# Optimization experiments

Measured on AMD Instinct MI355X. Metric: run time of the kernel, lower is better.

Reference implementation:

```python
import math
import jax, jax.numpy as jnp
import numpy as np

QDEPTH = 8
WIDTH = 32
HEIGHT = 32
PIXELS = WIDTH * HEIGHT          # 1024
WIRES = int(math.ceil(math.log2(PIXELS)))  # 10, and PIXELS == 2**WIRES exactly
BATCH = 2048


def setup_inputs() -> dict:
    key = jax.random.key(0)
    k1, k2 = jax.random.split(key)
    x = jax.random.normal(k1, (BATCH, 1, WIDTH, HEIGHT), dtype=jnp.float32)
    # torch.randn(weight_shape) * 0.4
    weights = jax.random.normal(k2, (QDEPTH, WIRES, 3), dtype=jnp.float32) * 0.4
    return {"x": x, "weights": weights, "reps": 1}


def _apply_1q(s, U, wire):
    # s: (batch, 2, 2, ..., 2); apply 2x2 unitary U on qubit `wire` (axis wire+1)
    ax = wire + 1
    s = jnp.moveaxis(s, ax, -1)
    s = s @ U.T                      # new[..., i] = sum_j U[i, j] * old[..., j]
    return jnp.moveaxis(s, -1, ax)


def _apply_cnot(s, ctrl, tgt):
    # flip target bit on the control==1 half of the state
    c_ax = ctrl + 1
    t_ax = tgt + 1
    s0 = jnp.take(s, 0, axis=c_ax)
    s1 = jnp.take(s, 1, axis=c_ax)
    t = t_ax - 1 if t_ax > c_ax else t_ax
    s1 = jnp.flip(s1, axis=t)
    return jnp.stack([s0, s1], axis=c_ax)


def _rot_matrix(phi, theta, omega):
    # qml.Rot = RZ(phi) -> RY(theta) -> RZ(omega)
    c = jnp.cos(theta * 0.5)
    sn = jnp.sin(theta * 0.5)
    ep = jnp.exp(-0.5j * (phi + omega))   # e^{-i(phi+omega)/2}
    em = jnp.exp(-0.5j * (phi - omega))   # e^{-i(phi-omega)/2}
    return jnp.stack([
        jnp.stack([ep * c, -jnp.conj(em) * sn]),
        jnp.stack([em * sn, jnp.conj(ep) * c]),
    ]).astype(jnp.complex64)


def _circuit(psi, weights, reps):
    # psi: (batch, 2**WIRES) complex64 normalized state
    b = psi.shape[0]
    s = psi.reshape((b,) + (2,) * WIRES)
    w = jnp.tanh(weights)                 # qw_map.tanh
    # StronglyEntanglingLayers default ranges: r_l = l % (wires-1) + 1
    ranges = [(l % (WIRES - 1)) + 1 for l in range(QDEPTH)]
    for _ in range(reps):
        for l in range(QDEPTH):
            for q in range(WIRES):
                U = _rot_matrix(w[l, q, 0], w[l, q, 1], w[l, q, 2])
                s = _apply_1q(s, U, q)
            r = ranges[l]
            for q in range(WIRES):
                s = _apply_cnot(s, q, (q + r) % WIRES)
    return s.reshape(b, 2 ** WIRES)


def reference(x, weights, reps):
    b = x.shape[0]
    v = x.reshape(b, PIXELS)                       # b 1 w h -> b (w h)
    old_norm = jnp.linalg.norm(v, axis=-1, keepdims=True)
    psi = (v / old_norm).astype(jnp.complex64)     # real amplitudes, zero imag
    out = _circuit(psi, weights, reps)
    out = out * old_norm.astype(jnp.complex64)
    return out.reshape(b, 1, WIDTH, HEIGHT)
```

## Files before the change

kernel.cpp:

```cpp
#include <hip/hip_runtime.h>
#include <math.h>


#define WIRES   10
#define NSTATE  1024
#define QDEPTH  8
#define NBATCH  2048
#define NGATES  (QDEPTH * WIRES)

typedef float v2f __attribute__((ext_vector_type(2)));
typedef unsigned int v2u __attribute__((ext_vector_type(2)));
static __device__ __forceinline__ v2f s2(float x) { return (v2f){x, x}; }

__device__ __forceinline__ int perm_g(int j, int r) {
#pragma unroll
    for (int q = WIRES - 1; q >= 0; --q) {
        const int cb = 9 - q;
        const int tb = 9 - ((q + r) % WIRES);
        j ^= ((j >> cb) & 1) << tb;
    }
    return j;
}

#if __has_builtin(__builtin_amdgcn_readlane)
static __device__ __forceinline__ int rli(int v, int idx) {
    return __builtin_amdgcn_readlane(v, idx);
}
#else
static __device__ __forceinline__ int rli(int v, int idx) {
    return __shfl(v, idx, 64);
}
#endif
static __device__ __forceinline__ float rlf(float v, int idx) {
    return __int_as_float(rli(__float_as_int(v), idx));
}

template<int CTRL>
__device__ __forceinline__ float dppmov(float x) {
    return __int_as_float(__builtin_amdgcn_update_dpp(
        0, __float_as_int(x), CTRL, 0xF, 0xF, true));
}
#define FX1(v)  dppmov<0xB1>(v)
#define FX2(v)  dppmov<0x4E>(v)
#define FX4(v)  dppmov<0x1B>(dppmov<0x141>(v))
#define FX8(v)  dppmov<0x128>(v)

#if __has_builtin(__builtin_amdgcn_permlane16_swap)
static __device__ __forceinline__ float pl16swap(float x) {
    const v2u r = __builtin_amdgcn_permlane16_swap(
        __float_as_uint(x), __float_as_uint(x), false, false);
    return __uint_as_float((threadIdx.x & 16) ? r.x : r.y);
}
#define FX16(v) pl16swap(v)
#else
#define FX16(v) __shfl_xor((v), 16, 64)
#endif

#if __has_builtin(__builtin_amdgcn_permlane32_swap)
static __device__ __forceinline__ float pl32swap(float x) {
    const v2u r = __builtin_amdgcn_permlane32_swap(
        __float_as_uint(x), __float_as_uint(x), false, false);
    return __uint_as_float((threadIdx.x & 32) ? r.x : r.y);
}
#define FX32(v) pl32swap(v)
#else
#define FX32(v) __shfl_xor((v), 32, 64)
#endif

__device__ __forceinline__ void gate_coeffs4(
    const float* __restrict__ w, int g, float (&c4)[4])
{
    const float phi   = tanhf(w[g * 3 + 0]);
    const float theta = tanhf(w[g * 3 + 1]);
    const float omega = tanhf(w[g * 3 + 2]);
    const float c  = cosf(theta * 0.5f);
    const float sn = sinf(theta * 0.5f);
    const float a  = 0.5f * (phi + omega);
    const float bb = 0.5f * (phi - omega);
    const float ca = cosf(a),  sa = sinf(a);
    const float cb = cosf(bb), sb = sinf(bb);
    c4[0] =  ca * c;
    c4[1] = -sa * c;
    c4[2] = -cb * sn;
    c4[3] = -sb * sn;
}

static __device__ __forceinline__ float sgnxor(float v, unsigned s) {
    return __uint_as_float(__float_as_uint(v) ^ s);
}

#define LOCAL_GATE(Q, MASK)                                                   \
    {                                                                         \
        const float u00r=getc(Q,0), u00i=getc(Q,1);                           \
        const float u01r=getc(Q,2), u01i=getc(Q,3);                           \
        _Pragma("unroll")                                                     \
        for (int k0 = 0; k0 < 8; ++k0) {                                      \
            if (k0 & (MASK)) continue;                                        \
            const int k1 = k0 | (MASK);                                       \
            const v2f a0r = zr[k0], a0i = zi[k0];                             \
            const v2f a1r = zr[k1], a1i = zi[k1];                             \
            zr[k0] = s2(u00r)*a0r - s2(u00i)*a0i + s2(u01r)*a1r - s2(u01i)*a1i;\
            zi[k0] = s2(u00r)*a0i + s2(u00i)*a0r + s2(u01r)*a1i + s2(u01i)*a1r;\
            zr[k1] = s2(u00r)*a1r + s2(u00i)*a1i - s2(u01r)*a0r - s2(u01i)*a0i;\
            zi[k1] = s2(u00r)*a1i - s2(u00i)*a1r - s2(u01r)*a0i + s2(u01i)*a0r;\
        }                                                                     \
    }

#define HSWAP_GATE(Q)                                                         \
    {                                                                         \
        const float u00r=getc(Q,0), u00i=getc(Q,1);                           \
        const float u01r=getc(Q,2), u01i=getc(Q,3);                           \
        const v2f pAr = s2(u00r);                                             \
        const v2f pAi = (v2f){u00i, -u00i};                                   \
        const v2f pBr = (v2f){u01r, -u01r};                                   \
        const v2f pBi = s2(u01i);                                             \
        _Pragma("unroll")                                                     \
        for (int k = 0; k < 8; ++k) {                                         \
            const v2f r  = zr[k], i = zi[k];                                  \
            const v2f rs = __builtin_shufflevector(r, r, 1, 0);               \
            const v2f is = __builtin_shufflevector(i, i, 1, 0);               \
            zr[k] = pAr*r - pAi*i + pBr*rs - pBi*is;                          \
            zi[k] = pAr*i + pAi*r + pBr*is + pBi*rs;                          \
        }                                                                     \
    }

#define LANE_GATE(Q, J, FETCH)                                                \
    {                                                                         \
        const float u00r=getc(Q,0), u00i=getc(Q,1);                           \
        const float u01r=getc(Q,2), u01i=getc(Q,3);                           \
        const unsigned sgn = ((unsigned)(lane >> (J)) & 1u) << 31;            \
        const float c0r = u00r,            c0i = sgnxor(u00i, sgn);           \
        const float c1r = sgnxor(u01r, sgn), c1i = u01i;                      \
        _Pragma("unroll")                                                     \
        for (int k = 0; k < 8; ++k) {                                         \
            v2f pr, pi;                                                       \
            pr.x = FETCH(zr[k].x); pr.y = FETCH(zr[k].y);                     \
            pi.x = FETCH(zi[k].x); pi.y = FETCH(zi[k].y);                     \
            const v2f sr = zr[k], si = zi[k];                                 \
            zr[k] = s2(c0r)*sr - s2(c0i)*si + s2(c1r)*pr - s2(c1i)*pi;        \
            zi[k] = s2(c0r)*si + s2(c0i)*sr + s2(c1r)*pi + s2(c1i)*pr;        \
        }                                                                     \
    }

template<typename GetC>
__device__ __forceinline__ void layer_body(
    v2f (&zr)[8], v2f (&zi)[8], GetC getc,
    const int G0, const int G1, const int G2, const int G3,
    const int ga, float* __restrict__ lds, const int lane)
{
    LOCAL_GATE(9, 1)
    LOCAL_GATE(8, 2)
    LOCAL_GATE(7, 4)
    HSWAP_GATE(6)
    LANE_GATE(5, 0, FX1)
    LANE_GATE(4, 1, FX2)
    LANE_GATE(3, 2, FX4)
    LANE_GATE(2, 3, FX8)
    LANE_GATE(1, 4, FX16)
    LANE_GATE(0, 5, FX32)

#pragma unroll
    for (int k = 0; k < 8; ++k) {
        const int w = k * 64 + lane;
        lds[w]        = zr[k].x;
        lds[w + 512]  = zr[k].y;
        lds[w + 1024] = zi[k].x;
        lds[w + 1536] = zi[k].y;
    }
    const int s01 = G0 ^ G1;
    const int gkt[8] = {0, G0, G1, s01, G2, G2 ^ G0, G2 ^ G1, G2 ^ s01};
#pragma unroll
    for (int k = 0; k < 8; ++k) {
        const int a0 = ga ^ gkt[k];
        const int a1 = a0 ^ G3;
        zr[k].x = lds[a0]; zi[k].x = lds[a0 + 1024];
        zr[k].y = lds[a1]; zi[k].y = lds[a1 + 1024];
    }
}

__global__ __launch_bounds__(64) void qsim_rl2(
    const float* __restrict__ x,
    const float* __restrict__ weights,
    float* __restrict__ out,
    const int interleaved)
{
    __shared__ float lds[2 * NSTATE];
    __shared__ int   gaT[QDEPTH * 64];

    const int lane = threadIdx.x;
    const int b    = blockIdx.x;

    for (int i = 0; i < (b & 7); ++i) __builtin_amdgcn_s_sleep(4);

    float cA[4], cB[4];
    gate_coeffs4(weights, lane, cA);
    gate_coeffs4(weights, 64 + (lane & 15), cB);

    int gv;
    {
        const int lg = (lane >> 2) & 7;
        const int bb = lane & 3;
        const int j  = perm_g(1 << bb, lg + 1);
        gv = ((j & 15) << 6) | (j >> 4);
    }
#pragma unroll
    for (int l = 0; l < QDEPTH; ++l) {
        const int j = perm_g(lane << 4, l + 1);
        gaT[l * 64 + lane] = ((j & 15) << 6) | (j >> 4);
    }

    v2f zr[8], zi[8];
    const float4* __restrict__ x4 =
        (const float4*)(x + ((size_t)b << 10) + (lane << 4));
    {
        const float4 v0 = x4[0], v1 = x4[1], v2 = x4[2], v3 = x4[3];
        zr[0].x=v0.x; zr[1].x=v0.y; zr[2].x=v0.z; zr[3].x=v0.w;
        zr[4].x=v1.x; zr[5].x=v1.y; zr[6].x=v1.z; zr[7].x=v1.w;
        zr[0].y=v2.x; zr[1].y=v2.y; zr[2].y=v2.z; zr[3].y=v2.w;
        zr[4].y=v3.x; zr[5].y=v3.y; zr[6].y=v3.z; zr[7].y=v3.w;
#pragma unroll
        for (int k = 0; k < 8; ++k) zi[k] = (v2f){0.f, 0.f};
    }

    int ga = gaT[lane];

#pragma unroll 1
    for (int l = 0; l < 6; ++l) {
        const int sb = l * 10;
        const int G0 = rli(gv, 4 * l + 0);
        const int G1 = rli(gv, 4 * l + 1);
        const int G2 = rli(gv, 4 * l + 2);
        const int G3 = rli(gv, 4 * l + 3);
        const int ga_nx = gaT[(l + 1) * 64 + lane];
        layer_body(zr, zi,
            [&](int q, int j) { return rlf(cA[j], sb + q); },
            G0, G1, G2, G3, ga, lds, lane);
        ga = ga_nx;
    }
    {
        const int G0 = rli(gv, 24), G1 = rli(gv, 25);
        const int G2 = rli(gv, 26), G3 = rli(gv, 27);
        const int ga_nx = gaT[7 * 64 + lane];
        layer_body(zr, zi,
            [&](int q, int j) {
                return (q < 4) ? rlf(cA[j], 60 + q) : rlf(cB[j], q - 4);
            },
            G0, G1, G2, G3, ga, lds, lane);
        ga = ga_nx;
    }
    {
        const int G0 = rli(gv, 28), G1 = rli(gv, 29);
        const int G2 = rli(gv, 30), G3 = rli(gv, 31);
        layer_body(zr, zi,
            [&](int q, int j) { return rlf(cB[j], 6 + q); },
            G0, G1, G2, G3, ga, lds, lane);
    }

    if (interleaved) {
        float2* __restrict__ o2 = (float2*)out;
        const size_t base = ((size_t)b << 10) + (lane << 4);
#pragma unroll
        for (int k = 0; k < 8; ++k) {
            o2[base + k]     = make_float2(zr[k].x, zi[k].x);
            o2[base + k + 8] = make_float2(zr[k].y, zi[k].y);
        }
    } else {
        float4* __restrict__ o4 = (float4*)(out + ((size_t)b << 10) + (lane << 4));
        o4[0] = make_float4(zr[0].x, zr[1].x, zr[2].x, zr[3].x);
        o4[1] = make_float4(zr[4].x, zr[5].x, zr[6].x, zr[7].x);
        o4[2] = make_float4(zr[0].y, zr[1].y, zr[2].y, zr[3].y);
        o4[3] = make_float4(zr[4].y, zr[5].y, zr[6].y, zr[7].y);
    }
}

extern "C" void kernel_launch(void* const* d_in, const int* in_sizes, int n_in,
                              void* d_out, int out_size, void* d_ws, size_t ws_size,
                              hipStream_t stream) {
    const float* x       = (const float*)d_in[0];
    const float* weights = (const float*)d_in[1];
    float* out = (float*)d_out;
    const int interleaved = (out_size >= 2 * NBATCH * NSTATE) ? 1 : 0;
    (void)d_ws; (void)ws_size;

    qsim_rl2<<<NBATCH, 64, 0, stream>>>(x, weights, out, interleaved);
}
```

Baseline: 105.9 us.

## Fuse wire-9 gate into LDS permutation reads and interleave last lane gate with stores

Moves the next layer's wire-9 local gate so it runs on register pairs immediately after each pair is read back from LDS. The last lane-shuffle gate is interleaved with the LDS stores. This lets LDS latency overlap with arithmetic instead of running as separate phases. The per-block staggered s_sleep at kernel start is also removed, and the layer loop is restructured so the first wire-9 gate is applied before it. The result relies on correct coefficient indexing for the peeled gates.

```diff
diff --git a/kernel.cpp b/kernel.cpp
--- a/kernel.cpp
+++ b/kernel.cpp
@@ -129,7 +129,7 @@
         const float u00r=getc(Q,0), u00i=getc(Q,1);                           \
         const float u01r=getc(Q,2), u01i=getc(Q,3);                           \
         const unsigned sgn = ((unsigned)(lane >> (J)) & 1u) << 31;            \
-        const float c0r = u00r,            c0i = sgnxor(u00i, sgn);           \
+        const float c0r = u00r,              c0i = sgnxor(u00i, sgn);         \
         const float c1r = sgnxor(u01r, sgn), c1i = u01i;                      \
         _Pragma("unroll")                                                     \
         for (int k = 0; k < 8; ++k) {                                         \
@@ -142,13 +142,23 @@
         }                                                                     \
     }
 
-template<typename GetC>
-__device__ __forceinline__ void layer_body(
-    v2f (&zr)[8], v2f (&zi)[8], GetC getc,
+#define W9_PAIR(KA)                                                           \
+    {                                                                         \
+        const int kA = (KA), kB = (KA) + 1;                                   \
+        const v2f a0r = zr[kA], a0i = zi[kA];                                 \
+        const v2f a1r = zr[kB], a1i = zi[kB];                                 \
+        zr[kA] = s2(n00r)*a0r - s2(n00i)*a0i + s2(n01r)*a1r - s2(n01i)*a1i;   \
+        zi[kA] = s2(n00r)*a0i + s2(n00i)*a0r + s2(n01r)*a1i + s2(n01i)*a1r;   \
+        zr[kB] = s2(n00r)*a1r + s2(n00i)*a1i - s2(n01r)*a0r - s2(n01i)*a0i;   \
+        zi[kB] = s2(n00r)*a1i - s2(n00i)*a1r - s2(n01r)*a0i + s2(n01i)*a0r;   \
+    }
+
+template<bool FUSE9, typename GetC, typename GetC9>
+__device__ __forceinline__ void layer_mid(
+    v2f (&zr)[8], v2f (&zi)[8], GetC getc, GetC9 getc9,
     const int G0, const int G1, const int G2, const int G3,
     const int ga, float* __restrict__ lds, const int lane)
 {
-    LOCAL_GATE(9, 1)
     LOCAL_GATE(8, 2)
     LOCAL_GATE(7, 4)
     HSWAP_GATE(6)
@@ -157,28 +167,56 @@
     LANE_GATE(3, 2, FX4)
     LANE_GATE(2, 3, FX8)
     LANE_GATE(1, 4, FX16)
-    LANE_GATE(0, 5, FX32)
-
-#pragma unroll
-    for (int k = 0; k < 8; ++k) {
-        const int w = k * 64 + lane;
-        lds[w]        = zr[k].x;
-        lds[w + 512]  = zr[k].y;
-        lds[w + 1024] = zi[k].x;
-        lds[w + 1536] = zi[k].y;
-    }
+
+    {
+        const float u00r=getc(0,0), u00i=getc(0,1);
+        const float u01r=getc(0,2), u01i=getc(0,3);
+        const unsigned sgn = ((unsigned)(lane >> 5) & 1u) << 31;
+        const float c0r = u00r,              c0i = sgnxor(u00i, sgn);
+        const float c1r = sgnxor(u01r, sgn), c1i = u01i;
+#pragma unroll
+        for (int k = 0; k < 8; ++k) {
+            v2f pr, pi;
+            pr.x = FX32(zr[k].x); pr.y = FX32(zr[k].y);
+            pi.x = FX32(zi[k].x); pi.y = FX32(zi[k].y);
+            const v2f sr = zr[k], si = zi[k];
+            zr[k] = s2(c0r)*sr - s2(c0i)*si + s2(c1r)*pr - s2(c1i)*pi;
+            zi[k] = s2(c0r)*si + s2(c0i)*sr + s2(c1r)*pi + s2(c1i)*pr;
+            const int w = k * 64 + lane;
+            lds[w]        = zr[k].x;
+            lds[w + 512]  = zr[k].y;
+            lds[w + 1024] = zi[k].x;
+            lds[w + 1536] = zi[k].y;
+        }
+    }
+
     const int s01 = G0 ^ G1;
     const int gkt[8] = {0, G0, G1, s01, G2, G2 ^ G0, G2 ^ G1, G2 ^ s01};
-#pragma unroll
-    for (int k = 0; k < 8; ++k) {
-        const int a0 = ga ^ gkt[k];
-        const int a1 = a0 ^ G3;
-        zr[k].x = lds[a0]; zi[k].x = lds[a0 + 1024];
-        zr[k].y = lds[a1]; zi[k].y = lds[a1 + 1024];
-    }
-}
-
-__global__ __launch_bounds__(64) void qsim_rl2(
+    if constexpr (FUSE9) {
+        const float n00r=getc9(0), n00i=getc9(1);
+        const float n01r=getc9(2), n01i=getc9(3);
+#pragma unroll
+        for (int k0 = 0; k0 < 8; k0 += 2) {
+            const int a0 = ga ^ gkt[k0],     a1 = a0 ^ G3;
+            zr[k0].x = lds[a0]; zi[k0].x = lds[a0 + 1024];
+            zr[k0].y = lds[a1]; zi[k0].y = lds[a1 + 1024];
+            const int b0 = ga ^ gkt[k0 + 1], b1 = b0 ^ G3;
+            zr[k0+1].x = lds[b0]; zi[k0+1].x = lds[b0 + 1024];
+            zr[k0+1].y = lds[b1]; zi[k0+1].y = lds[b1 + 1024];
+            W9_PAIR(k0)
+        }
+    } else {
+#pragma unroll
+        for (int k = 0; k < 8; ++k) {
+            const int a0 = ga ^ gkt[k];
+            const int a1 = a0 ^ G3;
+            zr[k].x = lds[a0]; zi[k].x = lds[a0 + 1024];
+            zr[k].y = lds[a1]; zi[k].y = lds[a1 + 1024];
+        }
+    }
+}
+
+__global__ __launch_bounds__(64) void qsim_pl(
     const float* __restrict__ x,
     const float* __restrict__ weights,
     float* __restrict__ out,
@@ -190,8 +228,6 @@
     const int lane = threadIdx.x;
     const int b    = blockIdx.x;
 
-    for (int i = 0; i < (b & 7); ++i) __builtin_amdgcn_s_sleep(4);
-
     float cA[4], cB[4];
     gate_coeffs4(weights, lane, cA);
     gate_coeffs4(weights, 64 + (lane & 15), cB);
@@ -199,8 +235,8 @@
     int gv;
     {
         const int lg = (lane >> 2) & 7;
-        const int bb = lane & 3;
-        const int j  = perm_g(1 << bb, lg + 1);
+        const int bbit = lane & 3;
+        const int j  = perm_g(1 << bbit, lg + 1);
         gv = ((j & 15) << 6) | (j >> 4);
     }
 #pragma unroll
@@ -222,37 +258,53 @@
         for (int k = 0; k < 8; ++k) zi[k] = (v2f){0.f, 0.f};
     }
 
-    int ga = gaT[lane];
+    {
+        const float n00r = rlf(cA[0], 9), n00i = rlf(cA[1], 9);
+        const float n01r = rlf(cA[2], 9), n01i = rlf(cA[3], 9);
+#pragma unroll
+        for (int k0 = 0; k0 < 8; k0 += 2) W9_PAIR(k0)
+    }
 
 #pragma unroll 1
-    for (int l = 0; l < 6; ++l) {
+    for (int l = 0; l < 5; ++l) {
         const int sb = l * 10;
         const int G0 = rli(gv, 4 * l + 0);
         const int G1 = rli(gv, 4 * l + 1);
         const int G2 = rli(gv, 4 * l + 2);
         const int G3 = rli(gv, 4 * l + 3);
-        const int ga_nx = gaT[(l + 1) * 64 + lane];
-        layer_body(zr, zi,
+        const int ga = gaT[l * 64 + lane];
+        layer_mid<true>(zr, zi,
             [&](int q, int j) { return rlf(cA[j], sb + q); },
+            [&](int j) { return rlf(cA[j], sb + 19); },
             G0, G1, G2, G3, ga, lds, lane);
-        ga = ga_nx;
+    }
+    {
+        const int G0 = rli(gv, 20), G1 = rli(gv, 21);
+        const int G2 = rli(gv, 22), G3 = rli(gv, 23);
+        const int ga = gaT[5 * 64 + lane];
+        layer_mid<true>(zr, zi,
+            [&](int q, int j) { return rlf(cA[j], 50 + q); },
+            [&](int j) { return rlf(cB[j], 5); },
+            G0, G1, G2, G3, ga, lds, lane);
     }
     {
         const int G0 = rli(gv, 24), G1 = rli(gv, 25);
         const int G2 = rli(gv, 26), G3 = rli(gv, 27);
-        const int ga_nx = gaT[7 * 64 + lane];
-        layer_body(zr, zi,
+        const int ga = gaT[6 * 64 + lane];
+        layer_mid<true>(zr, zi,
             [&](int q, int j) {
                 return (q < 4) ? rlf(cA[j], 60 + q) : rlf(cB[j], q - 4);
             },
+            [&](int j) { return rlf(cB[j], 15); },
             G0, G1, G2, G3, ga, lds, lane);
-        ga = ga_nx;
     }
     {
         const int G0 = rli(gv, 28), G1 = rli(gv, 29);
         const int G2 = rli(gv, 30), G3 = rli(gv, 31);
-        layer_body(zr, zi,
+        const int ga = gaT[7 * 64 + lane];
+        layer_mid<false>(zr, zi,
             [&](int q, int j) { return rlf(cB[j], 6 + q); },
+            [&](int j) { return 0.0f; },
             G0, G1, G2, G3, ga, lds, lane);
     }
 
@@ -282,5 +334,5 @@
     const int interleaved = (out_size >= 2 * NBATCH * NSTATE) ? 1 : 0;
     (void)d_ws; (void)ws_size;
 
-    qsim_rl2<<<NBATCH, 64, 0, stream>>>(x, weights, out, interleaved);
-}
+    qsim_pl<<<NBATCH, 64, 0, stream>>>(x, weights, out, interleaved);
+}
```

Result: no change. 104.9 us (-0.9%).
